# Performance work log

Measured on AMD Instinct MI355X. Metric: run time of the kernel, lower is better.

The kernel has to match this reference:

```python
import jax, jax.numpy as jnp
import numpy as np

B, T, C, H = 2, 2048, 1024, 16
HD = C // H          # head_dim = 64
RD = HD // 2         # rotary half-dim = 32


def _rope_tables(T, rd, base=10000.0):
    inv_freq = 1.0 / (base ** (np.arange(rd, dtype=np.float32) / rd))
    t = np.arange(T, dtype=np.float32)
    ang = np.outer(t, inv_freq)  # [T, rd]
    cos = np.cos(ang)[None, :, None, :]  # [1,T,1,rd]
    sin = np.sin(ang)[None, :, None, :]
    return jnp.asarray(cos), jnp.asarray(sin)


def setup_inputs() -> dict:
    key = jax.random.key(0)
    k1, k2, k3 = jax.random.split(key, 3)
    cos, sin = _rope_tables(T, RD)
    return {
        "x": jax.random.normal(k1, (B, T, C), dtype=jnp.float32),
        "cos": cos,
        "sin": sin,
        "W_qkv": jax.random.normal(k2, (C, C), dtype=jnp.float32) / np.sqrt(C),
        "W_proj": jax.random.normal(k3, (C, C), dtype=jnp.float32) / np.sqrt(C),
        "window_left": 512,
    }


def _apply_rotary(x, cos, sin):
    # x: [B,T,H,HD]
    x1, x2 = x[..., :RD], x[..., RD:]
    y1 = x1 * cos + x2 * sin
    y2 = -x1 * sin + x2 * cos
    return jnp.concatenate([y1, y2], axis=-1)


def _rms_norm(x):
    eps = jnp.finfo(x.dtype).eps
    ms = jnp.mean(jnp.square(x), axis=-1, keepdims=True)
    return x * jax.lax.rsqrt(ms + eps)


def reference(x, cos, sin, W_qkv, W_proj, window_left):
    Bx, Tx, Cx = x.shape
    scale = HD ** -0.5
    # tied QKV projection (single matmul)
    w = jnp.einsum("btc,cd->btd", x, W_qkv).reshape(Bx, Tx, H, HD)
    w = _apply_rotary(w, cos, sin)
    w = _rms_norm(w)                      # [B,T,H,HD]
    wq = jnp.transpose(w, (0, 2, 1, 3))    # [B,H,T,HD]
    dots = jnp.einsum("bhqd,bhkd->bhqk", wq, wq) * scale  # [B,H,T,T]
    # causal + sliding-window mask: allow 0 <= (q - k) <= window_left
    i = jnp.arange(Tx)[:, None]
    j = jnp.arange(Tx)[None, :]
    dist = i - j
    allowed = (dist >= 0) & ((window_left <= 0) | (dist <= window_left))
    dots = jnp.where(allowed, dots, -jnp.inf)
    attn = jax.nn.softmax(dots, axis=-1)
    out = jnp.einsum("bhqk,bhkd->bhqd", attn, wq)
    out = jnp.transpose(out, (0, 2, 1, 3)).reshape(Bx, Tx, Cx)
    return jnp.einsum("btc,cd->btd", out, W_proj)
```

## Files before the change

### kernel.cpp

```cpp
#include <hip/hip_runtime.h>
#include <hip/hip_bf16.h>

typedef __bf16 bf16_t;
typedef __bf16 bf16x4 __attribute__((ext_vector_type(4)));
typedef __bf16 bf16x8 __attribute__((ext_vector_type(8)));
typedef float f32x4 __attribute__((ext_vector_type(4)));

#define B_ 2
#define T_ 2048
#define C_ 1024
#define H_ 16
#define HD_ 64
#define RD_ 32
#define M_ (B_ * T_)

__global__ __launch_bounds__(256) void k_prep(const float* __restrict__ x,
                                              bf16_t* __restrict__ xb,
                                              const float* __restrict__ Wq,
                                              bf16_t* __restrict__ wqt,
                                              const float* __restrict__ Wp,
                                              bf16_t* __restrict__ wpt) {
    const int bid = blockIdx.x;
    if (bid < 4096) {
        int i = bid * 256 + threadIdx.x;
        float4 v = reinterpret_cast<const float4*>(x)[i];
        bf16x4 o;
        o[0] = (bf16_t)v.x; o[1] = (bf16_t)v.y; o[2] = (bf16_t)v.z; o[3] = (bf16_t)v.w;
        reinterpret_cast<bf16x4*>(xb)[i] = o;
    } else {
        __shared__ float tile[32][33];
        int b2 = bid - 4096;
        const float* W = (b2 < 1024) ? Wq : Wp;
        bf16_t* Wt = (b2 < 1024) ? wqt : wpt;
        b2 &= 1023;
        const int n0 = (b2 & 31) * 32, k0 = (b2 >> 5) * 32;
        const int tx = threadIdx.x & 31, ty = threadIdx.x >> 5;
        for (int i = ty; i < 32; i += 8)
            tile[i][tx] = W[(size_t)(k0 + i) * C_ + n0 + tx];
        __syncthreads();
        for (int i = ty; i < 32; i += 8)
            Wt[(size_t)(n0 + i) * C_ + k0 + tx] = (bf16_t)tile[tx][i];
    }
}

template <bool FUSED>
__global__ __launch_bounds__(256) void k_gemm(const bf16_t* __restrict__ A,
                                              const bf16_t* __restrict__ Bt,
                                              float* __restrict__ C,
                                              const float* __restrict__ ct,
                                              const float* __restrict__ st,
                                              bf16_t* __restrict__ qp,
                                              bf16_t* __restrict__ vp,
                                              int M, int N, int K) {
    constexpr int SMEM_BYTES = FUSED ? 52224 : 49152;
    __shared__ __align__(16) char smem[SMEM_BYTES];
    bf16_t* As = (bf16_t*)smem;
    bf16_t* Bs = (bf16_t*)(smem + 32768);
    const int tid = threadIdx.x;
    const int lane = tid & 63, w = tid >> 6;
    const int wr = w >> 1, wc = w & 1;
    const int g = lane >> 4, li = lane & 15;
    const int bid = blockIdx.x;
    const int work = (bid & 7) * 64 + (bid >> 3);
    const int bx = work & 15;
    const int by = work >> 4;
    const size_t rowA0 = (size_t)by * 128;
    const size_t colB0 = (size_t)bx * 64;
    const bf16_t* Ab = A + rowA0 * K;
    const bf16_t* Bb = Bt + colB0 * K;
    f32x4 acc[4][2] = {};

    const int lr = lane >> 3;
    const int swc = ((lane & 7) ^ lr) * 8;

    auto stage = [&](int buf, int k0) {
        bf16_t* Ad = As + buf * 8192 + (w * 8) * 64;
        bf16_t* Bd = Bs + buf * 4096 + (w * 8) * 64;
#pragma unroll
        for (int a = 0; a < 4; ++a) {
            const bf16_t* src = Ab + (size_t)(a * 32 + w * 8 + lr) * K + k0 + swc;
            __builtin_amdgcn_global_load_lds(
                (const __attribute__((address_space(1))) void*)src,
                (__attribute__((address_space(3))) void*)(Ad + a * 32 * 64), 16, 0, 0);
        }
#pragma unroll
        for (int bq = 0; bq < 2; ++bq) {
            const bf16_t* src = Bb + (size_t)(bq * 32 + w * 8 + lr) * K + k0 + swc;
            __builtin_amdgcn_global_load_lds(
                (const __attribute__((address_space(1))) void*)src,
                (__attribute__((address_space(3))) void*)(Bd + bq * 32 * 64), 16, 0, 0);
        }
    };

    stage(0, 0);
    __syncthreads();
    int cur = 0;
    const int NT = K >> 6;
    for (int kt = 0; kt < NT; ++kt) {
        if (kt < NT - 1) stage(cur ^ 1, (kt + 1) << 6);
        bf16x8 af[4][2], bfr[2][2];
#pragma unroll
        for (int i = 0; i < 4; ++i) {
            const int row = wr * 64 + i * 16 + li;
#pragma unroll
            for (int kk = 0; kk < 2; ++kk)
                af[i][kk] = *(const bf16x8*)(As + cur * 8192 + row * 64 +
                                             (((kk * 4 + g) ^ (li & 7)) * 8));
        }
#pragma unroll
        for (int j = 0; j < 2; ++j) {
            const int row = wc * 32 + j * 16 + li;
#pragma unroll
            for (int kk = 0; kk < 2; ++kk)
                bfr[j][kk] = *(const bf16x8*)(Bs + cur * 4096 + row * 64 +
                                              (((kk * 4 + g) ^ (li & 7)) * 8));
        }
#pragma unroll
        for (int i = 0; i < 4; ++i)
#pragma unroll
            for (int j = 0; j < 2; ++j)
#pragma unroll
                for (int kk = 0; kk < 2; ++kk)
                    acc[i][j] = __builtin_amdgcn_mfma_f32_16x16x32_bf16(
                        af[i][kk], bfr[j][kk], acc[i][j], 0, 0, 0);
        __syncthreads();
        cur ^= 1;
    }

    if constexpr (!FUSED) {
#pragma unroll
        for (int i = 0; i < 4; ++i)
#pragma unroll
            for (int j = 0; j < 2; ++j)
#pragma unroll
                for (int r = 0; r < 4; ++r) {
                    size_t row = rowA0 + wr * 64 + i * 16 + g * 4 + r;
                    size_t col = colB0 + wc * 32 + j * 16 + li;
                    C[row * N + col] = acc[i][j][r];
                }
    } else {
        float* ot = (float*)smem;
        bf16_t* qs = (bf16_t*)(smem + 34816);
#pragma unroll
        for (int i = 0; i < 4; ++i)
#pragma unroll
            for (int j = 0; j < 2; ++j)
#pragma unroll
                for (int r = 0; r < 4; ++r)
                    ot[(wr * 64 + i * 16 + g * 4 + r) * 68 + wc * 32 + j * 16 + li] =
                        acc[i][j][r];
        __syncthreads();
        const int bb = (int)(rowA0 >> 11);
        {
            const int row = tid >> 1, half = tid & 1;
            const int t = ((int)rowA0 + row) & 2047;
            const float* own = ot + row * 68 + half * 32;
            const float* par = ot + row * 68 + (half ^ 1) * 32;
            const float* cp = ct + (size_t)t * RD_;
            const float* sp = st + (size_t)t * RD_;
            float y[32];
            float sq = 0.f;
#pragma unroll
            for (int c4 = 0; c4 < 8; ++c4) {
                float4 xo = ((const float4*)own)[c4];
                float4 xp = ((const float4*)par)[c4];
                float4 cc = ((const float4*)cp)[c4];
                float4 ss = ((const float4*)sp)[c4];
                float* yy = y + c4 * 4;
                if (half == 0) {
                    yy[0] = xo.x * cc.x + xp.x * ss.x;
                    yy[1] = xo.y * cc.y + xp.y * ss.y;
                    yy[2] = xo.z * cc.z + xp.z * ss.z;
                    yy[3] = xo.w * cc.w + xp.w * ss.w;
                } else {
                    yy[0] = xo.x * cc.x - xp.x * ss.x;
                    yy[1] = xo.y * cc.y - xp.y * ss.y;
                    yy[2] = xo.z * cc.z - xp.z * ss.z;
                    yy[3] = xo.w * cc.w - xp.w * ss.w;
                }
                sq += yy[0] * yy[0] + yy[1] * yy[1] + yy[2] * yy[2] + yy[3] * yy[3];
            }
            sq += __shfl_xor(sq, 1);
            const float rn = rsqrtf(sq * (1.0f / 64.0f) + 1.1920929e-7f);
            bf16_t yb[32];
#pragma unroll
            for (int e = 0; e < 32; ++e) yb[e] = (bf16_t)(y[e] * rn);
            bf16_t* qpb = qp + ((size_t)(bb * H_ + bx) * 128 + (t >> 4)) * 1024;
#pragma unroll
            for (int c8 = 0; c8 < 4; ++c8) {
                const int chunk = (half * 4 + c8) * 16 + (t & 15);
                *(bf16x8*)(qpb + chunk * 8) = *(const bf16x8*)(yb + c8 * 8);
            }
#pragma unroll
            for (int e = 0; e < 32; ++e)
                qs[(half * 32 + e) * 136 + row] = yb[e];
        }
        __syncthreads();
        {
            const int d = tid >> 2, jc4 = tid & 3;
            const int tt0 = (int)((rowA0 & 2047) >> 6);
            bf16_t* vpb = vp + ((size_t)(bb * H_ + bx) * 32) * 4096;
#pragma unroll
            for (int c = 0; c < 4; ++c) {
                const int jc = jc4 * 4 + c;
                bf16x8 v8 = *(const bf16x8*)(qs + d * 136 + jc * 8);
                bf16_t* dst = vpb + (size_t)(tt0 + (jc >> 3)) * 4096 +
                              ((d >> 4) * 8 + (jc & 7)) * 128 + (d & 15) * 8;
                *(bf16x8*)dst = v8;
            }
        }
    }
}

__global__ __launch_bounds__(256, 2) void k_attn(const bf16_t* __restrict__ qp,
                                                 const bf16_t* __restrict__ vp,
                                                 bf16_t* __restrict__ aout,
                                                 const int* __restrict__ wlp) {
    __shared__ bf16_t pb[4][2][16][40];
    const int tid = threadIdx.x;
    const int lane = tid & 63, w = tid >> 6;
    const int g = lane >> 4, li = lane & 15;
    const int bid = blockIdx.x;
    const int work = (bid & 7) * 64 + (bid >> 3);
    const int tb = work & 15;
    const int h = (work >> 4) & 15;
    const int b = work >> 8;
    const int Q0 = tb * 128;
    const bf16_t* bq = qp + (size_t)(b * H_ + h) * 131072;
    const bf16_t* bv = vp + (size_t)(b * H_ + h) * 131072;
    const int wl = wlp[0];
    const int wle = (wl <= 0 || wl > T_) ? T_ : wl;
    const int qw = Q0 + w * 32;
    const int qgA = qw + li;
    const int qgB = qw + 16 + li;

    const int fo = (g * 16 + li) * 8;
    const int vo = g * 128 + li * 8;

    bf16x8 aqA0 = *(const bf16x8*)(bq + (size_t)(qw >> 4) * 1024 + fo);
    bf16x8 aqA1 = *(const bf16x8*)(bq + (size_t)(qw >> 4) * 1024 + fo + 512);
    bf16x8 aqB0 = *(const bf16x8*)(bq + (size_t)((qw >> 4) + 1) * 1024 + fo);
    bf16x8 aqB1 = *(const bf16x8*)(bq + (size_t)((qw >> 4) + 1) * 1024 + fo + 512);

    f32x4 oA[4] = {}, oB[4] = {};
    float mA = -1e30f, lA = 0.f, mB = -1e30f, lB = 0.f;
    const float SC = 0.125f * 1.44269504089f;

    const int kb0 = (qw > wle) ? ((qw - wle) >> 6) : 0;
    const int kb1 = qw >> 6;

#define SOFTMAX_G(S4, QG, M, L, O)                                                     \
    {                                                                                  \
        float mn = M;                                                                  \
        _Pragma("unroll") for (int nb = 0; nb < 4; ++nb)                               \
        _Pragma("unroll") for (int r = 0; r < 4; ++r) {                                \
            const int j = J0 + nb * 16 + g * 4 + r;                                    \
            const int dist = (QG) - j;                                                 \
            float x = S4[nb][r] * SC;                                                  \
            S4[nb][r] = (dist >= 0 && dist <= wle) ? x : -__builtin_inff();            \
            mn = fmaxf(mn, S4[nb][r]);                                                 \
        }                                                                              \
        mn = fmaxf(mn, __shfl_xor(mn, 16));                                            \
        mn = fmaxf(mn, __shfl_xor(mn, 32));                                            \
        const float al = exp2f(M - mn);                                                \
        M = mn;                                                                        \
        float la = 0.f;                                                                \
        _Pragma("unroll") for (int nb = 0; nb < 4; ++nb)                               \
        _Pragma("unroll") for (int r = 0; r < 4; ++r) {                                \
            float pv = exp2f(S4[nb][r] - M);                                           \
            S4[nb][r] = pv;                                                            \
            la += pv;                                                                  \
        }                                                                              \
        la += __shfl_xor(la, 16);                                                      \
        la += __shfl_xor(la, 32);                                                      \
        L = L * al + la;                                                               \
        float alq[4];                                                                  \
        _Pragma("unroll") for (int r = 0; r < 4; ++r) alq[r] = __shfl(al, g * 4 + r);  \
        _Pragma("unroll") for (int dnb = 0; dnb < 4; ++dnb)                            \
        _Pragma("unroll") for (int r = 0; r < 4; ++r) O[dnb][r] *= alq[r];             \
    }

    for (int kb = kb0; kb <= kb1; ++kb) {
        const int J0 = kb << 6;
        const bf16_t* kt = bq + (size_t)kb * 4096;
        const bf16_t* vt = bv + (size_t)kb * 4096;
        bf16x8 kf[2][4];
#pragma unroll
        for (int ks = 0; ks < 2; ++ks)
#pragma unroll
            for (int nb = 0; nb < 4; ++nb)
                kf[ks][nb] = *(const bf16x8*)(kt + nb * 1024 + ks * 512 + fo);
        f32x4 s4A[4] = {}, s4B[4] = {};
        __builtin_amdgcn_s_setprio(1);
#pragma unroll
        for (int ks = 0; ks < 2; ++ks)
#pragma unroll
            for (int nb = 0; nb < 4; ++nb) {
                bf16x8 aq0 = (ks == 0) ? aqA0 : aqA1;
                bf16x8 bq0 = (ks == 0) ? aqB0 : aqB1;
                s4A[nb] = __builtin_amdgcn_mfma_f32_16x16x32_bf16(kf[ks][nb], aq0,
                                                                  s4A[nb], 0, 0, 0);
                s4B[nb] = __builtin_amdgcn_mfma_f32_16x16x32_bf16(kf[ks][nb], bq0,
                                                                  s4B[nb], 0, 0, 0);
            }
        __builtin_amdgcn_s_setprio(0);
        bf16x8 vf[2][4];
#pragma unroll
        for (int ks = 0; ks < 2; ++ks)
#pragma unroll
            for (int dnb = 0; dnb < 4; ++dnb)
                vf[ks][dnb] = *(const bf16x8*)(vt + dnb * 1024 + ks * 512 + vo);

        SOFTMAX_G(s4A, qgA, mA, lA, oA)
        SOFTMAX_G(s4B, qgB, mB, lB, oB)

#pragma unroll
        for (int ks = 0; ks < 2; ++ks) {
#pragma unroll
            for (int nb2 = 0; nb2 < 2; ++nb2) {
                const int nb = ks * 2 + nb2;
                bf16x4 pkA, pkB;
                pkA[0] = (bf16_t)s4A[nb][0]; pkA[1] = (bf16_t)s4A[nb][1];
                pkA[2] = (bf16_t)s4A[nb][2]; pkA[3] = (bf16_t)s4A[nb][3];
                pkB[0] = (bf16_t)s4B[nb][0]; pkB[1] = (bf16_t)s4B[nb][1];
                pkB[2] = (bf16_t)s4B[nb][2]; pkB[3] = (bf16_t)s4B[nb][3];
                *reinterpret_cast<bf16x4*>(&pb[w][0][li][nb2 * 16 + g * 4]) = pkA;
                *reinterpret_cast<bf16x4*>(&pb[w][1][li][nb2 * 16 + g * 4]) = pkB;
            }
            bf16x8 paA = *reinterpret_cast<const bf16x8*>(&pb[w][0][li][g * 8]);
            bf16x8 paB = *reinterpret_cast<const bf16x8*>(&pb[w][1][li][g * 8]);
            __builtin_amdgcn_s_setprio(1);
#pragma unroll
            for (int dnb = 0; dnb < 4; ++dnb) {
                oA[dnb] = __builtin_amdgcn_mfma_f32_16x16x32_bf16(paA, vf[ks][dnb],
                                                                  oA[dnb], 0, 0, 0);
                oB[dnb] = __builtin_amdgcn_mfma_f32_16x16x32_bf16(paB, vf[ks][dnb],
                                                                  oB[dnb], 0, 0, 0);
            }
            __builtin_amdgcn_s_setprio(0);
        }
    }
#undef SOFTMAX_G

    const float rlA = 1.0f / lA, rlB = 1.0f / lB;
    float rlqA[4], rlqB[4];
#pragma unroll
    for (int r = 0; r < 4; ++r) {
        rlqA[r] = __shfl(rlA, g * 4 + r);
        rlqB[r] = __shfl(rlB, g * 4 + r);
    }
#pragma unroll
    for (int dnb = 0; dnb < 4; ++dnb)
#pragma unroll
        for (int r = 0; r < 4; ++r) {
            const size_t tA = (size_t)qw + g * 4 + r;
            const size_t tB = tA + 16;
            aout[((size_t)b * T_ + tA) * C_ + h * 64 + dnb * 16 + li] =
                (bf16_t)(oA[dnb][r] * rlqA[r]);
            aout[((size_t)b * T_ + tB) * C_ + h * 64 + dnb * 16 + li] =
                (bf16_t)(oB[dnb][r] * rlqB[r]);
        }
}

extern "C" void kernel_launch(void* const* d_in, const int* in_sizes, int n_in,
                              void* d_out, int out_size, void* d_ws, size_t ws_size,
                              hipStream_t stream) {
    const float* x     = (const float*)d_in[0];
    const float* ct    = (const float*)d_in[1];
    const float* st    = (const float*)d_in[2];
    const float* Wqkv  = (const float*)d_in[3];
    const float* Wproj = (const float*)d_in[4];
    const int*   wl    = (const int*)d_in[5];
    float* out = (float*)d_out;
    char* ws = (char*)d_ws;

    bf16_t* xb    = (bf16_t*)(ws);
    bf16_t* wqkvt = (bf16_t*)(ws + (8ull << 20));
    bf16_t* wprot = (bf16_t*)(ws + (10ull << 20));
    bf16_t* qp    = (bf16_t*)(ws + (12ull << 20));
    bf16_t* vp    = (bf16_t*)(ws + (20ull << 20));
    bf16_t* ao    = (bf16_t*)(ws + (28ull << 20));

    k_prep<<<dim3(6144), dim3(256), 0, stream>>>(x, xb, Wqkv, wqkvt, Wproj, wprot);
    k_gemm<true><<<dim3(512), dim3(256), 0, stream>>>(xb, wqkvt, nullptr, ct, st,
                                                      qp, vp, M_, C_, C_);
    k_attn<<<dim3(512), dim3(256), 0, stream>>>(qp, vp, ao, wl);
    k_gemm<false><<<dim3(512), dim3(256), 0, stream>>>(ao, wprot, out, nullptr, nullptr,
                                                       nullptr, nullptr, M_, C_, C_);
}
```

Measured before the change: 70.14 us.

## Skip masking on interior attention tiles, split K/V loads, remap fused GEMM tiles

The attention loop now checks whether a 64-key tile lies fully inside the causal sliding window and, if so, only scales the scores, skipping the per-element mask test. K and V fragments are loaded in two halves, interleaved with the MFMAs, to cut register pressure and overlap loads with compute. The fused GEMM gets a tile mapping per XCD that groups 4x16 blocks for better L2 reuse. The upper key-block bound changes to (qw+31)>>6, which may add or shift a boundary tile and needs to stay consistent with the mask.

```diff
diff --git a/kernel.cpp b/kernel.cpp
--- a/kernel.cpp
+++ b/kernel.cpp
@@ -61,9 +61,16 @@
     const int wr = w >> 1, wc = w & 1;
     const int g = lane >> 4, li = lane & 15;
     const int bid = blockIdx.x;
-    const int work = (bid & 7) * 64 + (bid >> 3);
-    const int bx = work & 15;
-    const int by = work >> 4;
+    int bx, by;
+    if constexpr (FUSED) {
+        const int xcd = bid & 7, i = bid >> 3;
+        bx = (xcd & 3) * 4 + (i & 3);
+        by = (xcd >> 2) * 16 + (i >> 2);
+    } else {
+        const int work = (bid & 7) * 64 + (bid >> 3);
+        bx = work & 15;
+        by = work >> 4;
+    }
     const size_t rowA0 = (size_t)by * 128;
     const size_t colB0 = (size_t)bx * 64;
     const bf16_t* Ab = A + rowA0 * K;
@@ -239,26 +246,34 @@
 
     bf16x8 aqA0 = *(const bf16x8*)(bq + (size_t)(qw >> 4) * 1024 + fo);
     bf16x8 aqA1 = *(const bf16x8*)(bq + (size_t)(qw >> 4) * 1024 + fo + 512);
-    bf16x8 aqB0 = *(const bf16x8*)(bq + (size_t)((qw >> 4) + 1) * 1024 + fo);
-    bf16x8 aqB1 = *(const bf16x8*)(bq + (size_t)((qw >> 4) + 1) * 1024 + fo + 512);
+    bf16x8 aqB0 = *(const bf16x8*)(bq + ((size_t)(qw >> 4) + 1) * 1024 + fo);
+    bf16x8 aqB1 = *(const bf16x8*)(bq + ((size_t)(qw >> 4) + 1) * 1024 + fo + 512);
 
     f32x4 oA[4] = {}, oB[4] = {};
     float mA = -1e30f, lA = 0.f, mB = -1e30f, lB = 0.f;
     const float SC = 0.125f * 1.44269504089f;
 
     const int kb0 = (qw > wle) ? ((qw - wle) >> 6) : 0;
-    const int kb1 = qw >> 6;
+    const int kb1 = (qw + 31) >> 6;
 
 #define SOFTMAX_G(S4, QG, M, L, O)                                                     \
     {                                                                                  \
         float mn = M;                                                                  \
-        _Pragma("unroll") for (int nb = 0; nb < 4; ++nb)                               \
-        _Pragma("unroll") for (int r = 0; r < 4; ++r) {                                \
-            const int j = J0 + nb * 16 + g * 4 + r;                                    \
-            const int dist = (QG) - j;                                                 \
-            float x = S4[nb][r] * SC;                                                  \
-            S4[nb][r] = (dist >= 0 && dist <= wle) ? x : -__builtin_inff();            \
-            mn = fmaxf(mn, S4[nb][r]);                                                 \
+        if (interior) {                                                                \
+            _Pragma("unroll") for (int nb = 0; nb < 4; ++nb)                           \
+            _Pragma("unroll") for (int r = 0; r < 4; ++r) {                            \
+                S4[nb][r] *= SC;                                                       \
+                mn = fmaxf(mn, S4[nb][r]);                                             \
+            }                                                                          \
+        } else {                                                                       \
+            _Pragma("unroll") for (int nb = 0; nb < 4; ++nb)                           \
+            _Pragma("unroll") for (int r = 0; r < 4; ++r) {                            \
+                const int j = J0 + nb * 16 + g * 4 + r;                                \
+                const int dist = (QG) - j;                                             \
+                float x = S4[nb][r] * SC;                                              \
+                S4[nb][r] = (dist >= 0 && dist <= wle) ? x : -__builtin_inff();        \
+                mn = fmaxf(mn, S4[nb][r]);                                             \
+            }                                                                          \
         }                                                                              \
         mn = fmaxf(mn, __shfl_xor(mn, 16));                                            \
         mn = fmaxf(mn, __shfl_xor(mn, 32));                                            \
@@ -284,41 +299,66 @@
         const int J0 = kb << 6;
         const bf16_t* kt = bq + (size_t)kb * 4096;
         const bf16_t* vt = bv + (size_t)kb * 4096;
-        bf16x8 kf[2][4];
-#pragma unroll
-        for (int ks = 0; ks < 2; ++ks)
-#pragma unroll
-            for (int nb = 0; nb < 4; ++nb)
-                kf[ks][nb] = *(const bf16x8*)(kt + nb * 1024 + ks * 512 + fo);
         f32x4 s4A[4] = {}, s4B[4] = {};
         __builtin_amdgcn_s_setprio(1);
-#pragma unroll
-        for (int ks = 0; ks < 2; ++ks)
+        {
+            bf16x8 kf[4];
+#pragma unroll
+            for (int nb = 0; nb < 4; ++nb)
+                kf[nb] = *(const bf16x8*)(kt + nb * 1024 + fo);
 #pragma unroll
             for (int nb = 0; nb < 4; ++nb) {
-                bf16x8 aq0 = (ks == 0) ? aqA0 : aqA1;
-                bf16x8 bq0 = (ks == 0) ? aqB0 : aqB1;
-                s4A[nb] = __builtin_amdgcn_mfma_f32_16x16x32_bf16(kf[ks][nb], aq0,
-                                                                  s4A[nb], 0, 0, 0);
-                s4B[nb] = __builtin_amdgcn_mfma_f32_16x16x32_bf16(kf[ks][nb], bq0,
-                                                                  s4B[nb], 0, 0, 0);
-            }
+                s4A[nb] = __builtin_amdgcn_mfma_f32_16x16x32_bf16(kf[nb], aqA0, s4A[nb], 0, 0, 0);
+                s4B[nb] = __builtin_amdgcn_mfma_f32_16x16x32_bf16(kf[nb], aqB0, s4B[nb], 0, 0, 0);
+            }
+#pragma unroll
+            for (int nb = 0; nb < 4; ++nb)
+                kf[nb] = *(const bf16x8*)(kt + nb * 1024 + 512 + fo);
+#pragma unroll
+            for (int nb = 0; nb < 4; ++nb) {
+                s4A[nb] = __builtin_amdgcn_mfma_f32_16x16x32_bf16(kf[nb], aqA1, s4A[nb], 0, 0, 0);
+                s4B[nb] = __builtin_amdgcn_mfma_f32_16x16x32_bf16(kf[nb], aqB1, s4B[nb], 0, 0, 0);
+            }
+        }
         __builtin_amdgcn_s_setprio(0);
-        bf16x8 vf[2][4];
-#pragma unroll
-        for (int ks = 0; ks < 2; ++ks)
-#pragma unroll
-            for (int dnb = 0; dnb < 4; ++dnb)
-                vf[ks][dnb] = *(const bf16x8*)(vt + dnb * 1024 + ks * 512 + vo);
-
+        bf16x8 vf0[4];
+#pragma unroll
+        for (int dnb = 0; dnb < 4; ++dnb)
+            vf0[dnb] = *(const bf16x8*)(vt + dnb * 1024 + vo);
+
+        const bool interior = (J0 + 63 <= qw) && (J0 >= qw + 31 - wle);
         SOFTMAX_G(s4A, qgA, mA, lA, oA)
         SOFTMAX_G(s4B, qgB, mB, lB, oB)
 
-#pragma unroll
-        for (int ks = 0; ks < 2; ++ks) {
+        {
 #pragma unroll
             for (int nb2 = 0; nb2 < 2; ++nb2) {
-                const int nb = ks * 2 + nb2;
+                bf16x4 pkA, pkB;
+                pkA[0] = (bf16_t)s4A[nb2][0]; pkA[1] = (bf16_t)s4A[nb2][1];
+                pkA[2] = (bf16_t)s4A[nb2][2]; pkA[3] = (bf16_t)s4A[nb2][3];
+                pkB[0] = (bf16_t)s4B[nb2][0]; pkB[1] = (bf16_t)s4B[nb2][1];
+                pkB[2] = (bf16_t)s4B[nb2][2]; pkB[3] = (bf16_t)s4B[nb2][3];
+                *reinterpret_cast<bf16x4*>(&pb[w][0][li][nb2 * 16 + g * 4]) = pkA;
+                *reinterpret_cast<bf16x4*>(&pb[w][1][li][nb2 * 16 + g * 4]) = pkB;
+            }
+            bf16x8 paA = *reinterpret_cast<const bf16x8*>(&pb[w][0][li][g * 8]);
+            bf16x8 paB = *reinterpret_cast<const bf16x8*>(&pb[w][1][li][g * 8]);
+            __builtin_amdgcn_s_setprio(1);
+#pragma unroll
+            for (int dnb = 0; dnb < 4; ++dnb) {
+                oA[dnb] = __builtin_amdgcn_mfma_f32_16x16x32_bf16(paA, vf0[dnb], oA[dnb], 0, 0, 0);
+                oB[dnb] = __builtin_amdgcn_mfma_f32_16x16x32_bf16(paB, vf0[dnb], oB[dnb], 0, 0, 0);
+            }
+            __builtin_amdgcn_s_setprio(0);
+        }
+        {
+            bf16x8 vf1[4];
+#pragma unroll
+            for (int dnb = 0; dnb < 4; ++dnb)
+                vf1[dnb] = *(const bf16x8*)(vt + dnb * 1024 + 512 + vo);
+#pragma unroll
+            for (int nb2 = 0; nb2 < 2; ++nb2) {
+                const int nb = 2 + nb2;
                 bf16x4 pkA, pkB;
                 pkA[0] = (bf16_t)s4A[nb][0]; pkA[1] = (bf16_t)s4A[nb][1];
                 pkA[2] = (bf16_t)s4A[nb][2]; pkA[3] = (bf16_t)s4A[nb][3];
@@ -332,10 +372,8 @@
             __builtin_amdgcn_s_setprio(1);
 #pragma unroll
             for (int dnb = 0; dnb < 4; ++dnb) {
-                oA[dnb] = __builtin_amdgcn_mfma_f32_16x16x32_bf16(paA, vf[ks][dnb],
-                                                                  oA[dnb], 0, 0, 0);
-                oB[dnb] = __builtin_amdgcn_mfma_f32_16x16x32_bf16(paB, vf[ks][dnb],
-                                                                  oB[dnb], 0, 0, 0);
+                oA[dnb] = __builtin_amdgcn_mfma_f32_16x16x32_bf16(paA, vf1[dnb], oA[dnb], 0, 0, 0);
+                oB[dnb] = __builtin_amdgcn_mfma_f32_16x16x32_bf16(paB, vf1[dnb], oB[dnb], 0, 0, 0);
             }
             __builtin_amdgcn_s_setprio(0);
         }
```

Measured after the change: 70.15 us. No clear change (+0.0%).
